# Performance work log

Hardware: AMD Instinct MI355X
Metric: run time of the kernel (lower is better)

## Reference

```python
import jax, jax.numpy as jnp
import numpy as np


def conv1x1(x, W, b=None):
    # x: (B,C,N), W: (O,C) -> (B,O,N)
    y = jnp.einsum('oc,bcn->bon', W, x)
    if b is not None:
        y = y + b[None, :, None]
    return y


def knn_idx(x, k):
    # x: (B,3,N); torch knn: topk of negative squared distance (self included)
    xx = jnp.sum(x * x, axis=1)                        # (B,N)
    inner = jnp.einsum('bcn,bcm->bnm', x, x)           # (B,N,N)
    neg_dist = 2.0 * inner - xx[:, :, None] - xx[:, None, :]
    return jax.lax.top_k(neg_dist, k)[1]               # (B,N,k) int32


def gather_neighbors(x, idx):
    # x: (B,C,N), idx: (B,N,k) -> (B,N,k,C)
    xt = jnp.swapaxes(x, 1, 2)                         # (B,N,C)
    return jax.vmap(lambda f, i: f[i])(xt, idx)


def local_maxpool(x, idx):
    # (B,C,N) -> (B,N,C): max over k neighbors
    return jnp.max(gather_neighbors(x, idx), axis=2)


def local_cov(pts, idx):
    # pts: (B,3,N) -> (B,12,N): xyz concat outer(nbr0, nbr1)
    nb = gather_neighbors(pts, idx)                    # (B,N,k,3)
    outer = nb[:, :, 0, :, None] * nb[:, :, 1, None, :]  # (B,N,3,3)
    B, N = outer.shape[0], outer.shape[1]
    outer = jnp.swapaxes(outer.reshape(B, N, 9), 1, 2)  # (B,9,N)
    return jnp.concatenate([pts, outer], axis=1)


def setup_inputs() -> dict:
    key = jax.random.key(0)
    ks = jax.random.split(key, 20)
    B, N, K, NF = 16, 2048, 16, 128
    s = 0.05
    inp = {
        'pts': jax.random.normal(ks[0], (B, N, 3), dtype=jnp.float32),
        'W_m1a': jax.random.normal(ks[1], (64, 12), dtype=jnp.float32) * s,
        'b_m1a': jnp.zeros((64,), jnp.float32),
        'W_m1b': jax.random.normal(ks[2], (64, 64), dtype=jnp.float32) * s,
        'b_m1b': jnp.zeros((64,), jnp.float32),
        'W_m1c': jax.random.normal(ks[3], (64, 64), dtype=jnp.float32) * s,
        'b_m1c': jnp.zeros((64,), jnp.float32),
        'W_lin1': jax.random.normal(ks[4], (64, 64), dtype=jnp.float32) * s,
        'b_lin1': jnp.zeros((64,), jnp.float32),
        'W_c1': jax.random.normal(ks[5], (128, 64), dtype=jnp.float32) * s,
        'b_c1': jnp.zeros((128,), jnp.float32),
        'W_lin2': jax.random.normal(ks[6], (128, 128), dtype=jnp.float32) * s,
        'b_lin2': jnp.zeros((128,), jnp.float32),
        'W_c2': jax.random.normal(ks[7], (1024, 128), dtype=jnp.float32) * s,
        'b_c2': jnp.zeros((1024,), jnp.float32),
        'W_m2a': jax.random.normal(ks[8], (512, 1024), dtype=jnp.float32) * s,
        'b_m2a': jnp.zeros((512,), jnp.float32),
        'W_m2b': jax.random.normal(ks[9], (512, 512), dtype=jnp.float32) * s,
        'b_m2b': jnp.zeros((512,), jnp.float32),
        'W_emb': jax.random.normal(ks[10], (NF, 512), dtype=jnp.float32) * s,
        'k': K,
    }
    return inp


def reference(pts, W_m1a, b_m1a, W_m1b, b_m1b, W_m1c, b_m1c, W_lin1, b_lin1,
              W_c1, b_c1, W_lin2, b_lin2, W_c2, b_c2, W_m2a, b_m2a,
              W_m2b, b_m2b, W_emb, k):
    p = jnp.swapaxes(pts, 1, 2)                        # (B,3,N)
    idx = knn_idx(p, k)                                # (B,N,k)
    x = local_cov(p, idx)                              # (B,12,N)
    x = jax.nn.relu(conv1x1(x, W_m1a, b_m1a))
    x = jax.nn.relu(conv1x1(x, W_m1b, b_m1b))
    x = jax.nn.relu(conv1x1(x, W_m1c, b_m1c))          # (B,64,N)
    # graph layer
    x = local_maxpool(x, idx)                          # (B,N,64)
    x = x @ W_lin1.T + b_lin1
    x = jnp.swapaxes(x, 1, 2)                          # (B,64,N)
    x = jax.nn.relu(conv1x1(x, W_c1, b_c1))            # (B,128,N)
    x = local_maxpool(x, idx)                          # (B,N,128)
    x = x @ W_lin2.T + b_lin2
    x = jnp.swapaxes(x, 1, 2)
    x = conv1x1(x, W_c2, b_c2)                         # (B,1024,N)
    x = jnp.max(x, axis=2, keepdims=True)              # (B,1024,1)
    x = jax.nn.relu(conv1x1(x, W_m2a, b_m2a))
    x = conv1x1(x, W_m2b, b_m2b)                       # (B,512,1)
    feat = jnp.swapaxes(x, 1, 2).reshape(x.shape[0], 512)
    return feat @ W_emb.T                              # (B,128)
```

## Files before the change

kernel.cpp:

```cpp
#include <hip/hip_runtime.h>
#include <math.h>

#define N_   2048
#define NPTS 32768

typedef __attribute__((ext_vector_type(8))) short short8;
typedef __attribute__((ext_vector_type(4))) float f32x4;
typedef unsigned long long u64;

__device__ __forceinline__ unsigned short f2bf(float f) {
  unsigned int u = __float_as_uint(f);
  return (unsigned short)((u + 0x7fffu + ((u >> 16) & 1u)) >> 16);
}
__device__ __forceinline__ float4 max4(float4 a, float4 b) {
  return make_float4(fmaxf(a.x,b.x), fmaxf(a.y,b.y), fmaxf(a.z,b.z), fmaxf(a.w,b.w));
}

__global__ __launch_bounds__(256) void k_prep2(const float* __restrict__ pts,
                                               const float* __restrict__ Wc2,
                                               float4* __restrict__ pts4,
                                               unsigned short* __restrict__ wb) {
  if (blockIdx.x < 128) {
    int P = blockIdx.x * 256 + threadIdx.x;
    float x = pts[P*3+0], y = pts[P*3+1], z = pts[P*3+2];
    float xx = __fadd_rn(__fadd_rn(__fmul_rn(x,x), __fmul_rn(y,y)), __fmul_rn(z,z));
    pts4[P] = make_float4(x, y, z, xx);
  } else {
    int i = ((blockIdx.x - 128) * 256 + threadIdx.x) * 4;
    float4 w = *(const float4*)&Wc2[i];
    *(ushort4*)&wb[i] = make_ushort4(f2bf(w.x), f2bf(w.y), f2bf(w.z), f2bf(w.w));
  }
}

#define KCAP 32
__global__ __launch_bounds__(256) void k_knn4(const float4* __restrict__ pts4,
                                              u64* __restrict__ pk) {
  __shared__ float4 cand[512];
  __shared__ u64 ring[KCAP+1][256];
  const int tid = threadIdx.x;
  const int qg  = blockIdx.x;
  const int ch  = blockIdx.y;
  const int P   = qg * 256 + tid;
  const float4* base = pts4 + ((P >> 11) << 11);
  const int j0 = ch << 9;
  for (int i = tid; i < 512; i += 256) cand[i] = base[j0 + i];
  const float4 q = base[P & (N_-1)];
  __syncthreads();

  u64 K[16];
#pragma unroll
  for (int t = 0; t < 16; ++t) K[t] = 0ull;
  u64 kmin = 0ull;
  int cnt = 0;

#define FLUSH4() do { \
    int s = 0; \
    u64 fk_next = ring[0][tid]; \
    while (__any(s < cnt)) { \
      u64 fk = (s < cnt) ? fk_next : 0ull; \
      fk_next = ring[s+1][tid]; \
      if (fk > kmin) { \
        _Pragma("unroll") \
        for (int t = 15; t > 0; --t) { \
          if (K[t] < fk) K[t] = (K[t-1] < fk) ? K[t-1] : fk; \
        } \
        if (K[0] < fk) K[0] = fk; \
        kmin = K[15]; \
      } \
      ++s; \
    } \
    cnt = 0; \
  } while (0)

  for (int jj = 0; jj < 512; jj += 4) {
    if (__any(cnt > KCAP - 4)) FLUSH4();
#pragma unroll
    for (int u = 0; u < 4; ++u) {
      float4 c = cand[jj + u];
      float inner = __fadd_rn(__fadd_rn(__fmul_rn(q.x,c.x), __fmul_rn(q.y,c.y)),
                              __fmul_rn(q.z,c.z));
      float dj = __fsub_rn(__fsub_rn(__fmul_rn(2.f, inner), q.w), c.w);
      unsigned int du = __float_as_uint(dj);
      unsigned int kd = du ^ (((unsigned int)((int)du >> 31)) | 0x80000000u);
      u64 key = ((u64)kd << 32) | (unsigned int)(~(j0 + jj + u));
      if (key > kmin) { ring[cnt][tid] = key; ++cnt; }
    }
  }
  FLUSH4();
#undef FLUSH4
#pragma unroll
  for (int t = 0; t < 16; ++t)
    pk[((size_t)P*4 + ch)*16 + t] = K[t];
}

__device__ __forceinline__ void kmerge16(const u64* a, const u64* b, u64* m) {
#pragma unroll
  for (int t = 0; t < 16; ++t) m[t] = (a[t] >= b[15-t]) ? a[t] : b[15-t];
#pragma unroll
  for (int dd = 8; dd >= 1; dd >>= 1)
#pragma unroll
    for (int i = 0; i < 16; ++i)
      if ((i & dd) == 0) {
        int j = i + dd;
        if (m[i] < m[j]) { u64 t_ = m[i]; m[i] = m[j]; m[j] = t_; }
      }
}

__global__ __launch_bounds__(256) void k_mergecov(const u64* __restrict__ pk,
                                                  const float4* __restrict__ pts4,
                                                  const float* __restrict__ W,
                                                  const float* __restrict__ bias,
                                                  int* __restrict__ idx,
                                                  float* __restrict__ act0) {
  __shared__ float Wl[64*12];
  __shared__ float bl[64];
  const int tid = threadIdx.x;
  for (int i = tid; i < 768; i += 256) Wl[i] = W[i];
  if (tid < 64) bl[tid] = bias[tid];
  __syncthreads();

  int P = blockIdx.x * 256 + tid;
  const u64* row = pk + (size_t)P * 64;
  u64 L0[16], L1[16], A[16], B[16], M[16];
#pragma unroll
  for (int t = 0; t < 16; ++t) { L0[t] = row[t]; L1[t] = row[16+t]; }
  kmerge16(L0, L1, A);
#pragma unroll
  for (int t = 0; t < 16; ++t) { L0[t] = row[32+t]; L1[t] = row[48+t]; }
  kmerge16(L0, L1, B);
  kmerge16(A, B, M);
#pragma unroll
  for (int t = 0; t < 16; ++t)
    idx[(size_t)P*16 + t] = (int)(~(unsigned int)(M[t] & 0xFFFFFFFFull));

  const int j0 = (int)(~(unsigned int)(M[0] & 0xFFFFFFFFull));
  const int j1 = (int)(~(unsigned int)(M[1] & 0xFFFFFFFFull));
  const float4* base = pts4 + ((P >> 11) << 11);
  float4 p  = base[P & (N_-1)];
  float4 n0 = base[j0];
  float4 n1 = base[j1];
  float f[12];
  f[0]=p.x; f[1]=p.y; f[2]=p.z;
  f[3]=n0.x*n1.x; f[4]=n0.x*n1.y; f[5]=n0.x*n1.z;
  f[6]=n0.y*n1.x; f[7]=n0.y*n1.y; f[8]=n0.y*n1.z;
  f[9]=n0.z*n1.x; f[10]=n0.z*n1.y; f[11]=n0.z*n1.z;
  float* out = act0 + (size_t)P*64;
  for (int o4 = 0; o4 < 64; o4 += 4) {
    float4 v; float* vv = (float*)&v;
#pragma unroll
    for (int u = 0; u < 4; ++u) {
      int o = o4 + u;
      float acc = bl[o];
#pragma unroll
      for (int ci = 0; ci < 12; ++ci) acc += Wl[o*12+ci] * f[ci];
      vv[u] = fmaxf(acc, 0.f);
    }
    *(float4*)&out[o4] = v;
  }
}

__global__ __launch_bounds__(256) void k_m1bc(const float* __restrict__ X,
                                              const float* __restrict__ W1, const float* __restrict__ b1,
                                              const float* __restrict__ W2, const float* __restrict__ b2,
                                              float* __restrict__ Y) {
  __shared__ __align__(16) float Wt[64][68];
  __shared__ __align__(16) float Xt[64][68];
  const int tid = threadIdx.x;
  const int p0  = blockIdx.x * 64;
  const int cg = (tid & 15) * 4;
  const int pg = (tid >> 4) * 4;
  for (int i = tid; i < 4096; i += 256) {
    int r = i >> 6, k = i & 63;
    Wt[k][r] = W1[(size_t)r*64 + k];
    Xt[k][r] = X[(size_t)(p0 + r)*64 + k];
  }
  __syncthreads();
  float acc[4][4] = {{0.f,0.f,0.f,0.f},{0.f,0.f,0.f,0.f},{0.f,0.f,0.f,0.f},{0.f,0.f,0.f,0.f}};
#pragma unroll
  for (int k = 0; k < 64; ++k) {
    float4 wv = *(const float4*)&Wt[k][cg];
    float4 xv = *(const float4*)&Xt[k][pg];
    const float wr[4] = {wv.x, wv.y, wv.z, wv.w};
    const float xr[4] = {xv.x, xv.y, xv.z, xv.w};
#pragma unroll
    for (int i = 0; i < 4; ++i)
#pragma unroll
      for (int j = 0; j < 4; ++j)
        acc[i][j] += wr[i] * xr[j];
  }
  __syncthreads();
  float4 bv1 = *(const float4*)&b1[cg];
  const float br1[4] = {bv1.x, bv1.y, bv1.z, bv1.w};
#pragma unroll
  for (int i = 0; i < 4; ++i) {
    float4 v;
    v.x = fmaxf(acc[i][0] + br1[i], 0.f);
    v.y = fmaxf(acc[i][1] + br1[i], 0.f);
    v.z = fmaxf(acc[i][2] + br1[i], 0.f);
    v.w = fmaxf(acc[i][3] + br1[i], 0.f);
    *(float4*)&Xt[cg + i][pg] = v;
  }
  for (int i = tid; i < 4096; i += 256) {
    int r = i >> 6, k = i & 63;
    Wt[k][r] = W2[(size_t)r*64 + k];
  }
  __syncthreads();
  float ac2[4][4] = {{0.f,0.f,0.f,0.f},{0.f,0.f,0.f,0.f},{0.f,0.f,0.f,0.f},{0.f,0.f,0.f,0.f}};
#pragma unroll
  for (int k = 0; k < 64; ++k) {
    float4 wv = *(const float4*)&Wt[k][cg];
    float4 xv = *(const float4*)&Xt[k][pg];
    const float wr[4] = {wv.x, wv.y, wv.z, wv.w};
    const float xr[4] = {xv.x, xv.y, xv.z, xv.w};
#pragma unroll
    for (int i = 0; i < 4; ++i)
#pragma unroll
      for (int j = 0; j < 4; ++j)
        ac2[i][j] += wr[i] * xr[j];
  }
  float4 bv2 = *(const float4*)&b2[cg];
  const float br2[4] = {bv2.x, bv2.y, bv2.z, bv2.w};
#pragma unroll
  for (int j = 0; j < 4; ++j) {
    float4 st; float* sv = (float*)&st;
#pragma unroll
    for (int i = 0; i < 4; ++i) sv[i] = fmaxf(ac2[i][j] + br2[i], 0.f);
    *(float4*)&Y[(size_t)(p0 + pg + j)*64 + cg] = st;
  }
}

__global__ __launch_bounds__(256) void k_lin1c1(const float* __restrict__ A,
                                                const int* __restrict__ idx,
                                                const float* __restrict__ Wl1, const float* __restrict__ bl1,
                                                const float* __restrict__ Wc1, const float* __restrict__ bc1,
                                                float* __restrict__ Y) {
  __shared__ __align__(16) float Wt[64][68];
  __shared__ __align__(16) float Xt[64][68];
  __shared__ int il[1024];
  const int tid = threadIdx.x;
  const int p0  = blockIdx.x * 64;
  const int cg = (tid & 15) * 4;
  const int pg = (tid >> 4) * 4;
  const int gr = tid >> 2, gk = (tid & 3) * 16;
  const float* Ab = A + (size_t)((p0 >> 11) << 11) * 64;
  *(int4*)&il[tid*4] = *(const int4*)&idx[(size_t)p0*16 + tid*4];
  for (int i = tid; i < 4096; i += 256) {
    int r = i >> 6, k = i & 63;
    Wt[k][r] = Wl1[(size_t)r*64 + k];
  }
  __syncthreads();
  {
    float4 mm[4];
#pragma unroll
    for (int u = 0; u < 4; ++u) mm[u] = make_float4(-INFINITY,-INFINITY,-INFINITY,-INFINITY);
    const int* ir = &il[gr*16];
#pragma unroll
    for (int nb = 0; nb < 16; ++nb) {
      int j = ir[nb];
      const float4* row = (const float4*)&Ab[(size_t)j*64 + gk];
      mm[0] = max4(mm[0], row[0]);
      mm[1] = max4(mm[1], row[1]);
      mm[2] = max4(mm[2], row[2]);
      mm[3] = max4(mm[3], row[3]);
    }
    const float* mf = (const float*)mm;
#pragma unroll
    for (int u = 0; u < 16; ++u) Xt[gk + u][gr] = mf[u];
  }
  __syncthreads();
  float acc[4][4] = {{0.f,0.f,0.f,0.f},{0.f,0.f,0.f,0.f},{0.f,0.f,0.f,0.f},{0.f,0.f,0.f,0.f}};
#pragma unroll
  for (int k = 0; k < 64; ++k) {
    float4 wv = *(const float4*)&Wt[k][cg];
    float4 xv = *(const float4*)&Xt[k][pg];
    const float wr[4] = {wv.x, wv.y, wv.z, wv.w};
    const float xr[4] = {xv.x, xv.y, xv.z, xv.w};
#pragma unroll
    for (int i = 0; i < 4; ++i)
#pragma unroll
      for (int j = 0; j < 4; ++j)
        acc[i][j] += wr[i] * xr[j];
  }
  __syncthreads();
  float4 bv = *(const float4*)&bl1[cg];
  const float br[4] = {bv.x, bv.y, bv.z, bv.w};
#pragma unroll
  for (int i = 0; i < 4; ++i) {
    float4 v;
    v.x = acc[i][0] + br[i];
    v.y = acc[i][1] + br[i];
    v.z = acc[i][2] + br[i];
    v.w = acc[i][3] + br[i];
    *(float4*)&Xt[cg + i][pg] = v;
  }
  for (int i = tid; i < 4096; i += 256) {
    int r = i >> 6, k = i & 63;
    Wt[k][r] = Wc1[(size_t)r*64 + k];
  }
  __syncthreads();
  float ac2[4][4] = {{0.f,0.f,0.f,0.f},{0.f,0.f,0.f,0.f},{0.f,0.f,0.f,0.f},{0.f,0.f,0.f,0.f}};
#pragma unroll
  for (int k = 0; k < 64; ++k) {
    float4 wv = *(const float4*)&Wt[k][cg];
    float4 xv = *(const float4*)&Xt[k][pg];
    const float wr[4] = {wv.x, wv.y, wv.z, wv.w};
    const float xr[4] = {xv.x, xv.y, xv.z, xv.w};
#pragma unroll
    for (int i = 0; i < 4; ++i)
#pragma unroll
      for (int j = 0; j < 4; ++j)
        ac2[i][j] += wr[i] * xr[j];
  }
  float4 bc0 = *(const float4*)&bc1[cg];
  const float bc0r[4] = {bc0.x, bc0.y, bc0.z, bc0.w};
#pragma unroll
  for (int j = 0; j < 4; ++j) {
    float4 st; float* sv = (float*)&st;
#pragma unroll
    for (int i = 0; i < 4; ++i) sv[i] = fmaxf(ac2[i][j] + bc0r[i], 0.f);
    *(float4*)&Y[(size_t)(p0 + pg + j)*128 + cg] = st;
  }
  __syncthreads();
  for (int i = tid; i < 4096; i += 256) {
    int r = i >> 6, k = i & 63;
    Wt[k][r] = Wc1[(size_t)(64 + r)*64 + k];
  }
  __syncthreads();
  float ac3[4][4] = {{0.f,0.f,0.f,0.f},{0.f,0.f,0.f,0.f},{0.f,0.f,0.f,0.f},{0.f,0.f,0.f,0.f}};
#pragma unroll
  for (int k = 0; k < 64; ++k) {
    float4 wv = *(const float4*)&Wt[k][cg];
    float4 xv = *(const float4*)&Xt[k][pg];
    const float wr[4] = {wv.x, wv.y, wv.z, wv.w};
    const float xr[4] = {xv.x, xv.y, xv.z, xv.w};
#pragma unroll
    for (int i = 0; i < 4; ++i)
#pragma unroll
      for (int j = 0; j < 4; ++j)
        ac3[i][j] += wr[i] * xr[j];
  }
  float4 bc4 = *(const float4*)&bc1[64 + cg];
  const float bc4r[4] = {bc4.x, bc4.y, bc4.z, bc4.w};
#pragma unroll
  for (int j = 0; j < 4; ++j) {
    float4 st; float* sv = (float*)&st;
#pragma unroll
    for (int i = 0; i < 4; ++i) sv[i] = fmaxf(ac3[i][j] + bc4r[i], 0.f);
    *(float4*)&Y[(size_t)(p0 + pg + j)*128 + 64 + cg] = st;
  }
}

__global__ __launch_bounds__(256) void k_lin2p(const float* __restrict__ A,
                                               const int* __restrict__ idx,
                                               const float* __restrict__ W,
                                               const float* __restrict__ bias,
                                               unsigned short* __restrict__ Y) {
  __shared__ __align__(16) float Wt[64][68];
  __shared__ __align__(16) float Xt[64][68];
  __shared__ int il[1024];
  const int tid = threadIdx.x;
  const int co0 = blockIdx.x * 64;
  const int p0  = blockIdx.y * 64;
  const int cg = (tid & 15) * 4;
  const int pg = (tid >> 4) * 4;
  const int gr = tid >> 2, gk = (tid & 3) * 16;
  const float* Ab = A + (size_t)((p0 >> 11) << 11) * 128;
  *(int4*)&il[tid*4] = *(const int4*)&idx[(size_t)p0*16 + tid*4];
  float acc[4][4] = {{0.f,0.f,0.f,0.f},{0.f,0.f,0.f,0.f},{0.f,0.f,0.f,0.f},{0.f,0.f,0.f,0.f}};
  for (int kt = 0; kt < 128; kt += 64) {
    __syncthreads();
    for (int i = tid; i < 4096; i += 256) {
      int r = i >> 6, k = i & 63;
      Wt[k][r] = W[(size_t)(co0 + r)*128 + kt + k];
    }
    {
      float4 mm[4];
#pragma unroll
      for (int u = 0; u < 4; ++u) mm[u] = make_float4(-INFINITY,-INFINITY,-INFINITY,-INFINITY);
      const int* ir = &il[gr*16];
#pragma unroll
      for (int nb = 0; nb < 16; ++nb) {
        int j = ir[nb];
        const float4* row = (const float4*)&Ab[(size_t)j*128 + kt + gk];
        mm[0] = max4(mm[0], row[0]);
        mm[1] = max4(mm[1], row[1]);
        mm[2] = max4(mm[2], row[2]);
        mm[3] = max4(mm[3], row[3]);
      }
      const float* mf = (const float*)mm;
#pragma unroll
      for (int u = 0; u < 16; ++u) Xt[gk + u][gr] = mf[u];
    }
    __syncthreads();
#pragma unroll
    for (int k = 0; k < 64; ++k) {
      float4 wv = *(const float4*)&Wt[k][cg];
      float4 xv = *(const float4*)&Xt[k][pg];
      const float wr[4] = {wv.x, wv.y, wv.z, wv.w};
      const float xr[4] = {xv.x, xv.y, xv.z, xv.w};
#pragma unroll
      for (int i = 0; i < 4; ++i)
#pragma unroll
        for (int j = 0; j < 4; ++j)
          acc[i][j] += wr[i] * xr[j];
    }
  }
  float4 bv = *(const float4*)&bias[co0 + cg];
  const float br[4] = {bv.x, bv.y, bv.z, bv.w};
#pragma unroll
  for (int j = 0; j < 4; ++j) {
    ushort4 st;
    st.x = f2bf(acc[0][j] + br[0]);
    st.y = f2bf(acc[1][j] + br[1]);
    st.z = f2bf(acc[2][j] + br[2]);
    st.w = f2bf(acc[3][j] + br[3]);
    *(ushort4*)&Y[(size_t)(p0 + pg + j)*128 + co0 + cg] = st;
  }
}

__global__ __launch_bounds__(256) void k_c2max(const unsigned short* __restrict__ X,
                                               const unsigned short* __restrict__ W,
                                               float* __restrict__ part) {
  __shared__ __align__(16) unsigned short Alds[128*136];
  __shared__ float red[128][4];
  const int tid  = threadIdx.x;
  const int wave = tid >> 6, lane = tid & 63;
  const int co0  = blockIdx.x * 128;
  const int p0   = blockIdx.y * 128;
  const int b    = blockIdx.z;
  const unsigned short* Xb = X + ((size_t)b * N_ + p0) * 128;

  for (int i = tid; i < 2048; i += 256) {
    int r = i >> 4, k8 = (i & 15) * 8;
    *(short8*)&Alds[r*136 + k8] = *(const short8*)&W[(size_t)(co0 + r)*128 + k8];
  }

  const int l16 = lane & 15, quad = lane >> 4;
  short8 b0[4], b1[4];
#pragma unroll
  for (int k0 = 0; k0 < 4; ++k0) {
    const int kk = k0*32 + quad*8;
    b0[k0] = *(const short8*)&Xb[(size_t)(wave*32 +      l16)*128 + kk];
    b1[k0] = *(const short8*)&Xb[(size_t)(wave*32 + 16 + l16)*128 + kk];
  }
  __syncthreads();

  f32x4 acc[8][2];
#pragma unroll
  for (int t = 0; t < 8; ++t) { acc[t][0] = (f32x4)0.f; acc[t][1] = (f32x4)0.f; }
#pragma unroll
  for (int k0 = 0; k0 < 4; ++k0) {
    const int kk = k0*32 + quad*8;
#pragma unroll
    for (int t = 0; t < 8; ++t) {
      short8 af = *(const short8*)&Alds[(t*16 + l16)*136 + kk];
      acc[t][0] = __builtin_amdgcn_mfma_f32_16x16x32_bf16(af, b0[k0], acc[t][0], 0, 0, 0);
      acc[t][1] = __builtin_amdgcn_mfma_f32_16x16x32_bf16(af, b1[k0], acc[t][1], 0, 0, 0);
    }
  }

#pragma unroll
  for (int t = 0; t < 8; ++t) {
#pragma unroll
    for (int r = 0; r < 4; ++r) {
      float m = fmaxf(acc[t][0][r], acc[t][1][r]);
      m = fmaxf(m, __shfl_xor(m, 1));
      m = fmaxf(m, __shfl_xor(m, 2));
      m = fmaxf(m, __shfl_xor(m, 4));
      m = fmaxf(m, __shfl_xor(m, 8));
      if (l16 == 0) red[t*16 + quad*4 + r][wave] = m;
    }
  }
  __syncthreads();
  if (tid < 128) {
    float m = fmaxf(fmaxf(red[tid][0], red[tid][1]), fmaxf(red[tid][2], red[tid][3]));
    part[((size_t)b*1024 + co0 + tid)*16 + blockIdx.y] = m;
  }
}

__global__ __launch_bounds__(256) void k_c2red(const float* __restrict__ part,
                                               const float* __restrict__ bias,
                                               float* __restrict__ g) {
  int i = blockIdx.x*256 + threadIdx.x;
  const float* p = part + (size_t)i*16;
  float m = -INFINITY;
#pragma unroll
  for (int t = 0; t < 16; ++t) m = fmaxf(m, p[t]);
  g[i] = m + bias[i & 1023];
}

__global__ __launch_bounds__(256) void k_m2a(const float* __restrict__ g,
                                             const float* __restrict__ Wa,
                                             const float* __restrict__ ba,
                                             float* __restrict__ h1) {
  const int tid = threadIdx.x;
  const int ks = tid & 1, b = (tid >> 1) & 15, o = blockIdx.x * 8 + (tid >> 5);
  const float4* wr = (const float4*)(Wa + (size_t)o*1024 + ks*512);
  const float4* gr = (const float4*)(g + (size_t)b*1024 + ks*512);
  float acc = 0.f;
#pragma unroll 8
  for (int i = 0; i < 128; ++i) {
    float4 w = wr[i], v = gr[i];
    acc += w.x*v.x + w.y*v.y + w.z*v.z + w.w*v.w;
  }
  acc += __shfl_xor(acc, 1);
  if (ks == 0) h1[(size_t)b*512 + o] = fmaxf(acc + ba[o], 0.f);
}

__global__ __launch_bounds__(256) void k_m2b(const float* __restrict__ h1,
                                             const float* __restrict__ Wb,
                                             const float* __restrict__ bb,
                                             float* __restrict__ h2) {
  const int tid = threadIdx.x;
  const int ks = tid & 1, b = (tid >> 1) & 15, o = blockIdx.x * 8 + (tid >> 5);
  const float4* wr = (const float4*)(Wb + (size_t)o*512 + ks*256);
  const float4* hr = (const float4*)(h1 + (size_t)b*512 + ks*256);
  float acc = 0.f;
#pragma unroll 8
  for (int i = 0; i < 64; ++i) {
    float4 w = wr[i], v = hr[i];
    acc += w.x*v.x + w.y*v.y + w.z*v.z + w.w*v.w;
  }
  acc += __shfl_xor(acc, 1);
  if (ks == 0) h2[(size_t)b*512 + o] = acc + bb[o];
}

__global__ __launch_bounds__(256) void k_emb(const float* __restrict__ h2,
                                             const float* __restrict__ We,
                                             float* __restrict__ out) {
  const int tid = threadIdx.x;
  const int ks = tid & 1, b = (tid >> 1) & 15, o = blockIdx.x * 8 + (tid >> 5);
  const float4* wr = (const float4*)(We + (size_t)o*512 + ks*256);
  const float4* hr = (const float4*)(h2 + (size_t)b*512 + ks*256);
  float acc = 0.f;
#pragma unroll 8
  for (int i = 0; i < 64; ++i) {
    float4 w = wr[i], v = hr[i];
    acc += w.x*v.x + w.y*v.y + w.z*v.z + w.w*v.w;
  }
  acc += __shfl_xor(acc, 1);
  if (ks == 0) out[(size_t)b*128 + o] = acc;
}

extern "C" void kernel_launch(void* const* d_in, const int* in_sizes, int n_in,
                              void* d_out, int out_size, void* d_ws, size_t ws_size,
                              hipStream_t stream) {
  const float* pts    = (const float*)d_in[0];
  const float* W_m1a  = (const float*)d_in[1];
  const float* b_m1a  = (const float*)d_in[2];
  const float* W_m1b  = (const float*)d_in[3];
  const float* b_m1b  = (const float*)d_in[4];
  const float* W_m1c  = (const float*)d_in[5];
  const float* b_m1c  = (const float*)d_in[6];
  const float* W_lin1 = (const float*)d_in[7];
  const float* b_lin1 = (const float*)d_in[8];
  const float* W_c1   = (const float*)d_in[9];
  const float* b_c1   = (const float*)d_in[10];
  const float* W_lin2 = (const float*)d_in[11];
  const float* b_lin2 = (const float*)d_in[12];
  const float* W_c2   = (const float*)d_in[13];
  const float* b_c2   = (const float*)d_in[14];
  const float* W_m2a  = (const float*)d_in[15];
  const float* b_m2a  = (const float*)d_in[16];
  const float* W_m2b  = (const float*)d_in[17];
  const float* b_m2b  = (const float*)d_in[18];
  const float* W_emb  = (const float*)d_in[19];
  float* out = (float*)d_out;

  char* ws = (char*)d_ws;
  const size_t MB = 1024*1024;
  float4* pts4 = (float4*)(ws + 0);
  unsigned short* wc2b = (unsigned short*)(ws + 512*1024);
  int*    idx  = (int*)  (ws + 1*MB);
  u64*    pk   = (u64*)  (ws + 3*MB);
  float*  act0 = (float*)(ws + 19*MB);
  float*  act1 = (float*)(ws + 3*MB);
  float*  act2 = (float*)(ws + 19*MB);
  unsigned short* act3b = (unsigned short*)(ws + 3*MB);
  float*  part = (float*)(ws + 12*MB);
  float*  gbuf = (float*)(ws + 13*MB);
  float*  h1   = (float*)(ws + 0);
  float*  h2   = (float*)(ws + 64*1024);

  k_prep2   <<<256, 256, 0, stream>>>(pts, W_c2, pts4, wc2b);
  k_knn4    <<<dim3(128, 4), 256, 0, stream>>>(pts4, pk);
  k_mergecov<<<128, 256, 0, stream>>>(pk, pts4, W_m1a, b_m1a, idx, act0);
  k_m1bc    <<<512, 256, 0, stream>>>(act0, W_m1b, b_m1b, W_m1c, b_m1c, act1);
  k_lin1c1  <<<512, 256, 0, stream>>>(act1, idx, W_lin1, b_lin1, W_c1, b_c1, act2);
  k_lin2p   <<<dim3(2,512), 256, 0, stream>>>(act2, idx, W_lin2, b_lin2, act3b);
  k_c2max   <<<dim3(8,16,16), 256, 0, stream>>>(act3b, wc2b, part);
  k_c2red   <<<64, 256, 0, stream>>>(part, b_c2, gbuf);
  k_m2a     <<<64, 256, 0, stream>>>(gbuf, W_m2a, b_m2a, h1);
  k_m2b     <<<64, 256, 0, stream>>>(h1, W_m2b, b_m2b, h2);
  k_emb     <<<16, 256, 0, stream>>>(h2, W_emb, out);
}
```

Measured before the change: 391.3 us.

## Split KNN candidate scan into 8 chunks with wider merge when workspace allows

Adds k_knn8, which splits each query's 2048 candidates into 8 chunks of 256 instead of 4 of 512. That doubles the grid to 1024 blocks for more parallelism and shortens each thread's serial top-k scan. A new k_mergecov8 merges eight sorted 16-lists per point with 128-thread blocks, and the covariance/conv code is factored into a shared helper. The path is chosen only when the workspace is at least 43 MB, and buffers are relocated to fit the larger partial-key array. The cost is more partial-key traffic and extra merge work per point.

```diff
diff --git a/kernel.cpp b/kernel.cpp
--- a/kernel.cpp
+++ b/kernel.cpp
@@ -93,6 +93,67 @@
     pk[((size_t)P*4 + ch)*16 + t] = K[t];
 }
 
+#define KCAP8 16
+__global__ __launch_bounds__(256) void k_knn8(const float4* __restrict__ pts4,
+                                              u64* __restrict__ pk) {
+  __shared__ float4 cand[256];
+  __shared__ u64 ring[KCAP8+1][256];
+  const int tid = threadIdx.x;
+  const int qg  = blockIdx.x;
+  const int ch  = blockIdx.y;
+  const int P   = qg * 256 + tid;
+  const float4* base = pts4 + ((P >> 11) << 11);
+  const int j0 = ch << 8;
+  cand[tid] = base[j0 + tid];
+  const float4 q = base[P & (N_-1)];
+  __syncthreads();
+
+  u64 K[16];
+#pragma unroll
+  for (int t = 0; t < 16; ++t) K[t] = 0ull;
+  u64 kmin = 0ull;
+  int cnt = 0;
+
+#define FLUSH8() do { \
+    int s = 0; \
+    u64 fk_next = ring[0][tid]; \
+    while (__any(s < cnt)) { \
+      u64 fk = (s < cnt) ? fk_next : 0ull; \
+      fk_next = ring[s+1][tid]; \
+      if (fk > kmin) { \
+        _Pragma("unroll") \
+        for (int t = 15; t > 0; --t) { \
+          if (K[t] < fk) K[t] = (K[t-1] < fk) ? K[t-1] : fk; \
+        } \
+        if (K[0] < fk) K[0] = fk; \
+        kmin = K[15]; \
+      } \
+      ++s; \
+    } \
+    cnt = 0; \
+  } while (0)
+
+  for (int jj = 0; jj < 256; jj += 4) {
+    if (__any(cnt > KCAP8 - 4)) FLUSH8();
+#pragma unroll
+    for (int u = 0; u < 4; ++u) {
+      float4 c = cand[jj + u];
+      float inner = __fadd_rn(__fadd_rn(__fmul_rn(q.x,c.x), __fmul_rn(q.y,c.y)),
+                              __fmul_rn(q.z,c.z));
+      float dj = __fsub_rn(__fsub_rn(__fmul_rn(2.f, inner), q.w), c.w);
+      unsigned int du = __float_as_uint(dj);
+      unsigned int kd = du ^ (((unsigned int)((int)du >> 31)) | 0x80000000u);
+      u64 key = ((u64)kd << 32) | (unsigned int)(~(j0 + jj + u));
+      if (key > kmin) { ring[cnt][tid] = key; ++cnt; }
+    }
+  }
+  FLUSH8();
+#undef FLUSH8
+#pragma unroll
+  for (int t = 0; t < 16; ++t)
+    pk[((size_t)P*8 + ch)*16 + t] = K[t];
+}
+
 __device__ __forceinline__ void kmerge16(const u64* a, const u64* b, u64* m) {
 #pragma unroll
   for (int t = 0; t < 16; ++t) m[t] = (a[t] >= b[15-t]) ? a[t] : b[15-t];
@@ -106,29 +167,11 @@
       }
 }
 
-__global__ __launch_bounds__(256) void k_mergecov(const u64* __restrict__ pk,
-                                                  const float4* __restrict__ pts4,
-                                                  const float* __restrict__ W,
-                                                  const float* __restrict__ bias,
-                                                  int* __restrict__ idx,
-                                                  float* __restrict__ act0) {
-  __shared__ float Wl[64*12];
-  __shared__ float bl[64];
-  const int tid = threadIdx.x;
-  for (int i = tid; i < 768; i += 256) Wl[i] = W[i];
-  if (tid < 64) bl[tid] = bias[tid];
-  __syncthreads();
-
-  int P = blockIdx.x * 256 + tid;
-  const u64* row = pk + (size_t)P * 64;
-  u64 L0[16], L1[16], A[16], B[16], M[16];
-#pragma unroll
-  for (int t = 0; t < 16; ++t) { L0[t] = row[t]; L1[t] = row[16+t]; }
-  kmerge16(L0, L1, A);
-#pragma unroll
-  for (int t = 0; t < 16; ++t) { L0[t] = row[32+t]; L1[t] = row[48+t]; }
-  kmerge16(L0, L1, B);
-  kmerge16(A, B, M);
+__device__ __forceinline__ void cov_m1a(int P, const u64* M,
+                                        const float4* __restrict__ pts4,
+                                        const float* Wl, const float* bl,
+                                        int* __restrict__ idx,
+                                        float* __restrict__ act0) {
 #pragma unroll
   for (int t = 0; t < 16; ++t)
     idx[(size_t)P*16 + t] = (int)(~(unsigned int)(M[t] & 0xFFFFFFFFull));
@@ -157,6 +200,66 @@
     }
     *(float4*)&out[o4] = v;
   }
+}
+
+__global__ __launch_bounds__(256) void k_mergecov(const u64* __restrict__ pk,
+                                                  const float4* __restrict__ pts4,
+                                                  const float* __restrict__ W,
+                                                  const float* __restrict__ bias,
+                                                  int* __restrict__ idx,
+                                                  float* __restrict__ act0) {
+  __shared__ float Wl[64*12];
+  __shared__ float bl[64];
+  const int tid = threadIdx.x;
+  for (int i = tid; i < 768; i += 256) Wl[i] = W[i];
+  if (tid < 64) bl[tid] = bias[tid];
+  __syncthreads();
+
+  int P = blockIdx.x * 256 + tid;
+  const u64* row = pk + (size_t)P * 64;
+  u64 L0[16], L1[16], A[16], B[16], M[16];
+#pragma unroll
+  for (int t = 0; t < 16; ++t) { L0[t] = row[t]; L1[t] = row[16+t]; }
+  kmerge16(L0, L1, A);
+#pragma unroll
+  for (int t = 0; t < 16; ++t) { L0[t] = row[32+t]; L1[t] = row[48+t]; }
+  kmerge16(L0, L1, B);
+  kmerge16(A, B, M);
+  cov_m1a(P, M, pts4, Wl, bl, idx, act0);
+}
+
+__global__ __launch_bounds__(128) void k_mergecov8(const u64* __restrict__ pk,
+                                                   const float4* __restrict__ pts4,
+                                                   const float* __restrict__ W,
+                                                   const float* __restrict__ bias,
+                                                   int* __restrict__ idx,
+                                                   float* __restrict__ act0) {
+  __shared__ float Wl[64*12];
+  __shared__ float bl[64];
+  const int tid = threadIdx.x;
+  for (int i = tid; i < 768; i += 128) Wl[i] = W[i];
+  if (tid < 64) bl[tid] = bias[tid];
+  __syncthreads();
+
+  int P = blockIdx.x * 128 + tid;
+  const u64* row = pk + (size_t)P * 128;
+  u64 X0[16], X1[16], A[16], B[16], E[16], M[16];
+#pragma unroll
+  for (int t = 0; t < 16; ++t) { X0[t] = row[t]; X1[t] = row[16+t]; }
+  kmerge16(X0, X1, A);
+#pragma unroll
+  for (int t = 0; t < 16; ++t) { X0[t] = row[32+t]; X1[t] = row[48+t]; }
+  kmerge16(X0, X1, B);
+  kmerge16(A, B, E);
+#pragma unroll
+  for (int t = 0; t < 16; ++t) { X0[t] = row[64+t]; X1[t] = row[80+t]; }
+  kmerge16(X0, X1, A);
+#pragma unroll
+  for (int t = 0; t < 16; ++t) { X0[t] = row[96+t]; X1[t] = row[112+t]; }
+  kmerge16(X0, X1, B);
+  kmerge16(A, B, X0);
+  kmerge16(E, X0, M);
+  cov_m1a(P, M, pts4, Wl, bl, idx, act0);
 }
 
 __global__ __launch_bounds__(256) void k_m1bc(const float* __restrict__ X,
@@ -569,22 +672,33 @@
 
   char* ws = (char*)d_ws;
   const size_t MB = 1024*1024;
+  const bool big = ws_size >= (size_t)43*MB;
+
   float4* pts4 = (float4*)(ws + 0);
   unsigned short* wc2b = (unsigned short*)(ws + 512*1024);
   int*    idx  = (int*)  (ws + 1*MB);
   u64*    pk   = (u64*)  (ws + 3*MB);
-  float*  act0 = (float*)(ws + 19*MB);
+  float*  act0 = big ? (float*)(ws + 35*MB)
+                     : (float*)(ws + 19*MB);
   float*  act1 = (float*)(ws + 3*MB);
   float*  act2 = (float*)(ws + 19*MB);
-  unsigned short* act3b = (unsigned short*)(ws + 3*MB);
-  float*  part = (float*)(ws + 12*MB);
-  float*  gbuf = (float*)(ws + 13*MB);
+  unsigned short* act3b = big ? (unsigned short*)(ws + 35*MB)
+                              : (unsigned short*)(ws + 3*MB);
+  float*  part = big ? (float*)(ws + 11*MB)
+                     : (float*)(ws + 12*MB);
+  float*  gbuf = big ? (float*)(ws + 12*MB)
+                     : (float*)(ws + 13*MB);
   float*  h1   = (float*)(ws + 0);
   float*  h2   = (float*)(ws + 64*1024);
 
   k_prep2   <<<256, 256, 0, stream>>>(pts, W_c2, pts4, wc2b);
-  k_knn4    <<<dim3(128, 4), 256, 0, stream>>>(pts4, pk);
-  k_mergecov<<<128, 256, 0, stream>>>(pk, pts4, W_m1a, b_m1a, idx, act0);
+  if (big) {
+    k_knn8     <<<dim3(128, 8), 256, 0, stream>>>(pts4, pk);
+    k_mergecov8<<<256, 128, 0, stream>>>(pk, pts4, W_m1a, b_m1a, idx, act0);
+  } else {
+    k_knn4     <<<dim3(128, 4), 256, 0, stream>>>(pts4, pk);
+    k_mergecov <<<128, 256, 0, stream>>>(pk, pts4, W_m1a, b_m1a, idx, act0);
+  }
   k_m1bc    <<<512, 256, 0, stream>>>(act0, W_m1b, b_m1b, W_m1c, b_m1c, act1);
   k_lin1c1  <<<512, 256, 0, stream>>>(act1, idx, W_lin1, b_lin1, W_c1, b_c1, act2);
   k_lin2p   <<<dim3(2,512), 256, 0, stream>>>(act2, idx, W_lin2, b_lin2, act3b);
```

Result: slower. 400.7 us (+2.4%).
